# Kernel optimization log

Hardware: AMD Instinct MI355X
Metric: run time of the kernel (lower is better)

The kernel has to match this reference:

```python
import jax, jax.numpy as jnp
import numpy as np

B, T, C = 4, 2048, 2048
N_HEAD = 16
N_KV_HEAD = 4
N_REP = N_HEAD // N_KV_HEAD  # 4
HD = C // N_HEAD             # 128
FC_MULT = 1.0
EPS = 1e-12


def l2norm(x):
    return x / (jnp.linalg.norm(x, axis=-1, keepdims=True) + EPS)


def setup_inputs() -> dict:
    key = jax.random.key(0)
    k1, k2, k3, k4 = jax.random.split(key, 4)
    s = 1.0 / np.sqrt(C)
    return {
        "x": jax.random.normal(k1, (B, T, C), dtype=jnp.float32),
        "Wq": jax.random.normal(k2, (C, C), dtype=jnp.float32) * s,
        "Wkv": jax.random.normal(k3, (C, 2 * C // N_REP), dtype=jnp.float32) * s,
        "Wproj": jax.random.normal(k4, (C, C), dtype=jnp.float32) * s,
    }


def reference(x, Wq, Wkv, Wproj):
    kv_dim = C // N_REP  # 512
    q = FC_MULT * (x @ Wq)                     # [B,T,C]
    kv = FC_MULT * (x @ Wkv)                   # [B,T,2*kv_dim]
    k, v = kv[..., :kv_dim], kv[..., kv_dim:]
    # L2 prenorm over full projection dims (before head split), as in module
    q = l2norm(q)
    k = l2norm(k)
    # split heads; GQA without materializing repeated K/V
    q = q.reshape(B, T, N_KV_HEAD, N_REP, HD)  # [B,T,G,R,H]
    k = k.reshape(B, T, N_KV_HEAD, HD)         # [B,S,G,H]
    v = v.reshape(B, T, N_KV_HEAD, HD)
    scale = 1.0 / np.sqrt(HD)
    scores = jnp.einsum('btgrh,bsgh->bgrts', q, k) * scale  # [B,G,R,T,S]
    causal = jnp.tril(jnp.ones((T, T), dtype=bool))
    scores = jnp.where(causal, scores, -jnp.inf)
    att = jax.nn.softmax(scores, axis=-1)
    y = jnp.einsum('bgrts,bsgh->btgrh', att, v)  # [B,T,G,R,H]
    y = y.reshape(B, T, C)
    return FC_MULT * (y @ Wproj)
```

## Files before the change

kernel.cpp:

```cpp
#include <hip/hip_runtime.h>
#include <hip/hip_bf16.h>
#include <math.h>

#define B_   4
#define T_   2048
#define C_   2048
#define NH_  16
#define HD_  128
#define KVD_ 1024

typedef __attribute__((ext_vector_type(4))) float f32x4;
typedef __attribute__((ext_vector_type(16))) float f32x16;
typedef __attribute__((ext_vector_type(8))) short bf16x8;
typedef __attribute__((ext_vector_type(4))) unsigned int u32x4;

__device__ __forceinline__ void async_copy16(const __hip_bfloat16* g, __hip_bfloat16* l) {
  __builtin_amdgcn_global_load_lds((const __attribute__((address_space(1))) void*)g,
                                   (__attribute__((address_space(3))) void*)l,
                                   16, 0, 0);
}

__device__ __forceinline__ float bf2f(__hip_bfloat16 h) { return __bfloat162float(h); }

__device__ __forceinline__ unsigned int pkbf(float a, float b) {
  float2 f2; f2.x = a; f2.y = b;
  __hip_bfloat162 h2 = __float22bfloat162_rn(f2);
  return *reinterpret_cast<unsigned int*>(&h2);
}

__global__ __launch_bounds__(256) void f32_to_bf16_k(const float* __restrict__ src,
                                                     __hip_bfloat16* __restrict__ dst, int n4) {
  int i = blockIdx.x * 256 + threadIdx.x;
  if (i >= n4) return;
  float4 f = ((const float4*)src)[i];
  __hip_bfloat16 o[4] = {__float2bfloat16(f.x), __float2bfloat16(f.y),
                         __float2bfloat16(f.z), __float2bfloat16(f.w)};
  *(uint2*)(dst + (size_t)i * 4) = *(uint2*)o;
}

__global__ __launch_bounds__(256) void transpose_f32_bf16_k(const float* __restrict__ W,
                                                            __hip_bfloat16* __restrict__ WT,
                                                            int K, int N) {
  __shared__ float tile[32][33];
  int bx = blockIdx.x * 32;
  int by = blockIdx.y * 32;
  int tx = threadIdx.x, ty = threadIdx.y;
  for (int i = ty; i < 32; i += 8)
    tile[i][tx] = W[(size_t)(by + i) * N + (bx + tx)];
  __syncthreads();
  for (int i = ty; i < 32; i += 8)
    WT[(size_t)(bx + i) * K + (by + tx)] = __float2bfloat16(tile[tx][i]);
}

__global__ __launch_bounds__(256) void vtrans_k(const __hip_bfloat16* __restrict__ kv,
                                                __hip_bfloat16* __restrict__ vt) {
  __shared__ __hip_bfloat16 tile[32][33];
  int bg = blockIdx.z;
  int d0 = blockIdx.y * 32;
  int t0 = blockIdx.x * 32;
  int tx = threadIdx.x, ty = threadIdx.y;
  int b = bg >> 2, g = bg & 3;
  const __hip_bfloat16* src = kv + (size_t)b * T_ * KVD_ + 512 + g * HD_;
  for (int i = ty; i < 32; i += 8)
    tile[i][tx] = src[(size_t)(t0 + i) * KVD_ + d0 + tx];
  __syncthreads();
  __hip_bfloat16* dst = vt + (size_t)bg * HD_ * T_;
  int txp = (tx & ~12) | ((tx & 4) << 1) | ((tx & 8) >> 1);
  for (int i = ty; i < 32; i += 8)
    dst[(size_t)(d0 + i) * T_ + t0 + txp] = tile[tx][i];
}

template<int PER>
__global__ __launch_bounds__(256) void rownorm_k(__hip_bfloat16* __restrict__ buf,
                                                 int stride, float extra) {
  const int tid = threadIdx.x;
  __hip_bfloat16* p = buf + (size_t)blockIdx.x * stride;
  float v[PER];
  float ss = 0.f;
  #pragma unroll
  for (int e = 0; e < PER; ++e) { v[e] = bf2f(p[tid + e * 256]); ss += v[e] * v[e]; }
  #pragma unroll
  for (int off = 32; off >= 1; off >>= 1) ss += __shfl_xor(ss, off, 64);
  __shared__ float wsum[4];
  if ((tid & 63) == 0) wsum[tid >> 6] = ss;
  __syncthreads();
  float tot = wsum[0] + wsum[1] + wsum[2] + wsum[3];
  float sc = extra / (sqrtf(tot) + 1e-12f);
  #pragma unroll
  for (int e = 0; e < PER; ++e) p[tid + e * 256] = __float2bfloat16(v[e] * sc);
}

template<typename OutT>
__global__ __launch_bounds__(256) void gemm_bt_k(const __hip_bfloat16* __restrict__ A,
                                                 const __hip_bfloat16* __restrict__ BT,
                                                 OutT* __restrict__ Cc,
                                                 int M, int N, int K) {
  __shared__ alignas(16) __hip_bfloat16 As[128 * 32];
  __shared__ alignas(16) __hip_bfloat16 Bs[128 * 32];
  const int tid = threadIdx.x;
  const int bm = blockIdx.y * 128;
  const int bn = blockIdx.x * 128;
  const int wave = tid >> 6, lane = tid & 63;
  const int wr = (wave >> 1) * 64, wc = (wave & 1) * 64;
  const int lm = lane & 15, lk = (lane >> 4) * 8;
  const size_t Kz = (size_t)K;
  const __hip_bfloat16* a0 = A + (size_t)(bm + (tid >> 2)) * Kz + (size_t)((tid & 3) * 8);
  const __hip_bfloat16* b0 = BT + (size_t)(bn + (tid >> 2)) * Kz + (size_t)((tid & 3) * 8);
  const __hip_bfloat16* a1 = a0 + 64 * Kz;
  const __hip_bfloat16* b1 = b0 + 64 * Kz;
  f32x4 acc[4][4] = {};
  for (int k0 = 0; k0 < K; k0 += 32) {
    async_copy16(a0 + k0, As + tid * 8);
    async_copy16(a1 + k0, As + 2048 + tid * 8);
    async_copy16(b0 + k0, Bs + tid * 8);
    async_copy16(b1 + k0, Bs + 2048 + tid * 8);
    __syncthreads();
    bf16x8 af[4], bfr[4];
    #pragma unroll
    for (int t = 0; t < 4; ++t) {
      af[t]  = *(const bf16x8*)(As + (wr + t * 16 + lm) * 32 + lk);
      bfr[t] = *(const bf16x8*)(Bs + (wc + t * 16 + lm) * 32 + lk);
    }
    #pragma unroll
    for (int mt = 0; mt < 4; ++mt)
      #pragma unroll
      for (int nt = 0; nt < 4; ++nt)
        acc[mt][nt] = __builtin_amdgcn_mfma_f32_16x16x32_bf16(af[mt], bfr[nt], acc[mt][nt], 0, 0, 0);
    __syncthreads();
  }
  const int r0 = (lane >> 4) * 4;
  #pragma unroll
  for (int mt = 0; mt < 4; ++mt)
    #pragma unroll
    for (int nt = 0; nt < 4; ++nt)
      #pragma unroll
      for (int r = 0; r < 4; ++r) {
        int gr = bm + wr + mt * 16 + r0 + r;
        int gc = bn + wc + nt * 16 + lm;
        float v = acc[mt][nt][r];
        if constexpr (__is_same(OutT, float))
          Cc[(size_t)gr * N + gc] = v;
        else
          Cc[(size_t)gr * N + gc] = __float2bfloat16(v);
      }
}

__global__ __launch_bounds__(256, 2) void attn_k(const __hip_bfloat16* __restrict__ q,
                                                 const __hip_bfloat16* __restrict__ kv,
                                                 const __hip_bfloat16* __restrict__ vt,
                                                 __hip_bfloat16* __restrict__ y) {
  const int pp = blockIdx.x;
  const int h  = blockIdx.y;
  const int b  = blockIdx.z;
  const int g  = h >> 2;
  const int tid = threadIdx.x;
  const int wave = tid >> 6, lane = tid & 63;
  const int l31 = lane & 31, hi = lane >> 5;

  __shared__ alignas(16) __hip_bfloat16 Ks[2][64 * 128];
  __shared__ alignas(16) __hip_bfloat16 Vts[2][128 * 64];

  const __hip_bfloat16* kb = kv + (size_t)b * T_ * KVD_ + g * HD_;
  const __hip_bfloat16* vb = vt + (size_t)(b * 4 + g) * HD_ * T_;

  auto stage = [&](int buf, int jt) {
    const size_t j1 = (size_t)jt * 64;
    #pragma unroll
    for (int e = 0; e < 4; ++e) {
      int idx = tid + e * 256;
      int row = idx >> 4, c = idx & 15;
      async_copy16(kb + (j1 + row) * KVD_ + ((c ^ (row & 15)) * 8), Ks[buf] + idx * 8);
    }
    #pragma unroll
    for (int e = 0; e < 4; ++e) {
      int idx = tid + e * 256;
      int row = idx >> 3, c = idx & 7;
      async_copy16(vb + (size_t)row * T_ + j1 + ((c ^ (row & 7)) * 8), Vts[buf] + idx * 8);
    }
  };

  stage(0, 0);

  #pragma unroll
  for (int seg = 0; seg < 2; ++seg) {
    const int qt = seg ? pp : (15 - pp);
    const int qbase = qt * 128 + wave * 32;
    const int qmax = qbase + 31;
    const int ntiles = 2 * qt + 2;

    const __hip_bfloat16* qrow = q + ((size_t)b * T_ + qbase + l31) * C_ + h * HD_;
    bf16x8 qf[8];
    #pragma unroll
    for (int kc = 0; kc < 8; ++kc)
      qf[kc] = *(const bf16x8*)(qrow + kc * 16 + hi * 8);

    __syncthreads();

    f32x16 o_acc[4] = {};
    float l_acc = 0.f;

    for (int it = 0; it < ntiles; ++it) {
      const int cur = it & 1;
      if (it + 1 < ntiles) stage(cur ^ 1, it + 1);
      const int j0 = it * 64;
      if (j0 <= qmax) {
        f32x16 st0 = {}, st1 = {};
        __builtin_amdgcn_s_setprio(1);
        #pragma unroll
        for (int kc = 0; kc < 8; ++kc) {
          const int cs0 = (((2 * kc + hi) ^ (l31 & 15)) * 8);
          bf16x8 k0 = *(const bf16x8*)(Ks[cur] + l31 * 128 + cs0);
          bf16x8 k1 = *(const bf16x8*)(Ks[cur] + (32 + l31) * 128 + cs0);
          st0 = __builtin_amdgcn_mfma_f32_32x32x16_bf16(k0, qf[kc], st0, 0, 0, 0);
          st1 = __builtin_amdgcn_mfma_f32_32x32x16_bf16(k1, qf[kc], st1, 0, 0, 0);
        }
        __builtin_amdgcn_s_setprio(0);
        const int qd = qbase + l31 - j0;
        if (j0 + 63 <= qbase) {
          #pragma unroll
          for (int r = 0; r < 16; ++r) {
            float p0 = __expf(st0[r]);
            float p1 = __expf(st1[r]);
            st0[r] = p0; st1[r] = p1;
            l_acc += p0 + p1;
          }
        } else {
          #pragma unroll
          for (int r = 0; r < 16; ++r) {
            const int ofs = (r & 3) + 8 * (r >> 2) + 4 * hi;
            float p0 = (ofs <= qd) ? __expf(st0[r]) : 0.f;
            float p1 = (ofs + 32 <= qd) ? __expf(st1[r]) : 0.f;
            st0[r] = p0; st1[r] = p1;
            l_acc += p0 + p1;
          }
        }
        unsigned int W[8][2];
        #pragma unroll
        for (int q4 = 0; q4 < 4; ++q4) {
          W[q4][0]     = pkbf(st0[4 * q4 + 0], st0[4 * q4 + 1]);
          W[q4][1]     = pkbf(st0[4 * q4 + 2], st0[4 * q4 + 3]);
          W[4 + q4][0] = pkbf(st1[4 * q4 + 0], st1[4 * q4 + 1]);
          W[4 + q4][1] = pkbf(st1[4 * q4 + 2], st1[4 * q4 + 3]);
        }
        __builtin_amdgcn_s_setprio(1);
        #pragma unroll
        for (int kc = 0; kc < 4; ++kc) {
          u32x4 pw;
          pw[0] = W[2 * kc][0]; pw[1] = W[2 * kc][1];
          pw[2] = W[2 * kc + 1][0]; pw[3] = W[2 * kc + 1][1];
          bf16x8 pf = __builtin_bit_cast(bf16x8, pw);
          const int csv = (((2 * kc + hi) ^ (l31 & 7)) * 8);
          #pragma unroll
          for (int ct = 0; ct < 4; ++ct) {
            bf16x8 vf = *(const bf16x8*)(Vts[cur] + (ct * 32 + l31) * 64 + csv);
            o_acc[ct] = __builtin_amdgcn_mfma_f32_32x32x16_bf16(pf, vf, o_acc[ct], 0, 0, 0);
          }
        }
        __builtin_amdgcn_s_setprio(0);
      }
      __syncthreads();
    }

    if (seg == 0) stage(0, 0);

    float lsum = l_acc + __shfl_xor(l_acc, 32, 64);
    float oinv[16];
    #pragma unroll
    for (int r = 0; r < 16; ++r) {
      int row = (r & 3) + 8 * (r >> 2) + 4 * hi;
      oinv[r] = 1.0f / __shfl(lsum, row, 64);
    }
    __hip_bfloat16* yb = y + ((size_t)b * T_ + qbase) * C_ + h * HD_ + l31;
    #pragma unroll
    for (int ct = 0; ct < 4; ++ct)
      #pragma unroll
      for (int r = 0; r < 16; ++r) {
        int row = (r & 3) + 8 * (r >> 2) + 4 * hi;
        yb[(size_t)row * C_ + ct * 32] = __float2bfloat16(o_acc[ct][r] * oinv[r]);
      }
  }
}

extern "C" void kernel_launch(void* const* d_in, const int* in_sizes, int n_in,
                              void* d_out, int out_size, void* d_ws, size_t ws_size,
                              hipStream_t stream) {
  (void)in_sizes; (void)n_in; (void)out_size; (void)ws_size;
  const float* x     = (const float*)d_in[0];
  const float* Wq    = (const float*)d_in[1];
  const float* Wkv   = (const float*)d_in[2];
  const float* Wproj = (const float*)d_in[3];
  char* ws = (char*)d_ws;
  __hip_bfloat16* xb     = (__hip_bfloat16*)(ws);
  __hip_bfloat16* WqT    = (__hip_bfloat16*)(ws + 33554432);
  __hip_bfloat16* WkvT   = (__hip_bfloat16*)(ws + 41943040);
  __hip_bfloat16* WprojT = (__hip_bfloat16*)(ws + 46137344);
  __hip_bfloat16* qn     = (__hip_bfloat16*)(ws + 54525952);
  __hip_bfloat16* kvb    = (__hip_bfloat16*)(ws + 88080384);
  __hip_bfloat16* y      = xb;
  __hip_bfloat16* vt     = (__hip_bfloat16*)d_out;
  float* out             = (float*)d_out;

  f32_to_bf16_k<<<16384, 256, 0, stream>>>(x, xb, 4194304);
  transpose_f32_bf16_k<<<dim3(64, 64), dim3(32, 8), 0, stream>>>(Wq, WqT, 2048, 2048);
  transpose_f32_bf16_k<<<dim3(32, 64), dim3(32, 8), 0, stream>>>(Wkv, WkvT, 2048, 1024);
  transpose_f32_bf16_k<<<dim3(64, 64), dim3(32, 8), 0, stream>>>(Wproj, WprojT, 2048, 2048);
  gemm_bt_k<__hip_bfloat16><<<dim3(16, 64), 256, 0, stream>>>(xb, WqT, qn, 8192, 2048, 2048);
  gemm_bt_k<__hip_bfloat16><<<dim3(8, 64), 256, 0, stream>>>(xb, WkvT, kvb, 8192, 1024, 2048);
  rownorm_k<8><<<8192, 256, 0, stream>>>(qn, 2048, 0.08838834764831845f);
  rownorm_k<2><<<8192, 256, 0, stream>>>(kvb, 1024, 1.0f);
  vtrans_k<<<dim3(64, 4, 16), dim3(32, 8), 0, stream>>>(kvb, vt);
  attn_k<<<dim3(8, 16, 4), 256, 0, stream>>>(qn, kvb, vt, y);
  gemm_bt_k<float><<<dim3(16, 64), 256, 0, stream>>>(y, WprojT, out, 8192, 2048, 2048);
}
```

Before: 546.8 us.

## Replace GEMM with triple-buffered 128x256 tile kernel using async LDS prefetch

Replaces the single-buffered 128x128x32 bf16 GEMM with a 512-thread kernel that computes 128x256 tiles with K-step 64. It triple-buffers the LDS tiles via global_load_lds prefetching two steps ahead, and uses an XOR-swizzled LDS layout to avoid bank conflicts. It also splits the MFMA work into two halves, interleaving B-tile loads between them, and raises wave priority while the MFMAs run. The goal is to hide global memory latency and remove the barrier stalls of the old kernel. The cost is about 144KB of LDS per block and hand-written vmcnt waits that have to match the number of issued copies.

```diff
diff --git a/kernel.cpp b/kernel.cpp
--- a/kernel.cpp
+++ b/kernel.cpp
@@ -91,53 +91,114 @@
 }
 
 template<typename OutT>
-__global__ __launch_bounds__(256) void gemm_bt_k(const __hip_bfloat16* __restrict__ A,
-                                                 const __hip_bfloat16* __restrict__ BT,
-                                                 OutT* __restrict__ Cc,
-                                                 int M, int N, int K) {
-  __shared__ alignas(16) __hip_bfloat16 As[128 * 32];
-  __shared__ alignas(16) __hip_bfloat16 Bs[128 * 32];
-  const int tid = threadIdx.x;
-  const int bm = blockIdx.y * 128;
-  const int bn = blockIdx.x * 128;
+__global__ __launch_bounds__(512, 2) void gemm3_k(const __hip_bfloat16* __restrict__ A,
+                                                  const __hip_bfloat16* __restrict__ BT,
+                                                  OutT* __restrict__ Cc,
+                                                  int M, int N, int K) {
+  __shared__ alignas(16) __hip_bfloat16 As[3][128 * 64];
+  __shared__ alignas(16) __hip_bfloat16 Bs[3][256 * 64];
+  const int tid  = threadIdx.x;
+  const int bm   = blockIdx.y * 128;
+  const int bn   = blockIdx.x * 256;
   const int wave = tid >> 6, lane = tid & 63;
-  const int wr = (wave >> 1) * 64, wc = (wave & 1) * 64;
-  const int lm = lane & 15, lk = (lane >> 4) * 8;
+  const int wm = wave >> 2, wn = wave & 3;
+  const int lm = lane & 15, quad = lane >> 4;
   const size_t Kz = (size_t)K;
-  const __hip_bfloat16* a0 = A + (size_t)(bm + (tid >> 2)) * Kz + (size_t)((tid & 3) * 8);
-  const __hip_bfloat16* b0 = BT + (size_t)(bn + (tid >> 2)) * Kz + (size_t)((tid & 3) * 8);
-  const __hip_bfloat16* a1 = a0 + 64 * Kz;
-  const __hip_bfloat16* b1 = b0 + 64 * Kz;
+  const int NT = K >> 6;
+
+  const int srow = tid >> 3;
+  const int csw  = ((tid & 7) ^ (srow & 7)) * 8;
+  const __hip_bfloat16* aSrc0 = A  + (size_t)(bm + srow) * Kz + csw;
+  const __hip_bfloat16* aSrc1 = A  + (size_t)(bm + 64 + srow) * Kz + csw;
+  const __hip_bfloat16* bSrc0 = BT + (size_t)(bn + srow) * Kz + csw;
+  const __hip_bfloat16* bSrc1 = BT + (size_t)(bn + 64 + srow) * Kz + csw;
+  const __hip_bfloat16* bSrc2 = BT + (size_t)(bn + 128 + srow) * Kz + csw;
+  const __hip_bfloat16* bSrc3 = BT + (size_t)(bn + 192 + srow) * Kz + csw;
+
+  auto stageA = [&](int slot, int koff) {
+    async_copy16(aSrc0 + koff, As[slot] + tid * 8);
+    async_copy16(aSrc1 + koff, As[slot] + (512 + tid) * 8);
+  };
+  auto stageB0 = [&](int slot, int koff) {
+    async_copy16(bSrc0 + koff, Bs[slot] + tid * 8);
+  };
+  auto stageB123 = [&](int slot, int koff) {
+    async_copy16(bSrc1 + koff, Bs[slot] + (512 + tid) * 8);
+    async_copy16(bSrc2 + koff, Bs[slot] + (1024 + tid) * 8);
+    async_copy16(bSrc3 + koff, Bs[slot] + (1536 + tid) * 8);
+  };
+
+  const int ch0 = ((quad) ^ (lm & 7)) * 8;
+  const int ch1 = ((4 + quad) ^ (lm & 7)) * 8;
+  const int arow = wm * 64 + lm;
+  const int brow = wn * 64 + lm;
+
   f32x4 acc[4][4] = {};
-  for (int k0 = 0; k0 < K; k0 += 32) {
-    async_copy16(a0 + k0, As + tid * 8);
-    async_copy16(a1 + k0, As + 2048 + tid * 8);
-    async_copy16(b0 + k0, Bs + tid * 8);
-    async_copy16(b1 + k0, Bs + 2048 + tid * 8);
-    __syncthreads();
-    bf16x8 af[4], bfr[4];
-    #pragma unroll
-    for (int t = 0; t < 4; ++t) {
-      af[t]  = *(const bf16x8*)(As + (wr + t * 16 + lm) * 32 + lk);
-      bfr[t] = *(const bf16x8*)(Bs + (wc + t * 16 + lm) * 32 + lk);
-    }
-    #pragma unroll
-    for (int mt = 0; mt < 4; ++mt)
+
+  stageA(0, 0); stageB0(0, 0); stageB123(0, 0);
+  if (NT > 1) { stageA(1, 64); stageB0(1, 64); stageB123(1, 64); }
+
+  int s = 0;
+  for (int t = 0; t < NT; ++t) {
+    const int sn = (s + 2 > 2) ? (s - 1) : (s + 2);
+    const bool pre = (t + 2) < NT;
+    const int koff = (t + 2) * 64;
+    if (t + 1 < NT) asm volatile("s_waitcnt vmcnt(6)" ::: "memory");
+    else            asm volatile("s_waitcnt vmcnt(0)" ::: "memory");
+    __builtin_amdgcn_s_barrier();
+    bf16x8 af[4][2], bf0[2][2];
+    #pragma unroll
+    for (int mf = 0; mf < 4; ++mf) {
+      af[mf][0] = *(const bf16x8*)(As[s] + (arow + mf * 16) * 64 + ch0);
+      af[mf][1] = *(const bf16x8*)(As[s] + (arow + mf * 16) * 64 + ch1);
+    }
+    #pragma unroll
+    for (int nf = 0; nf < 2; ++nf) {
+      bf0[nf][0] = *(const bf16x8*)(Bs[s] + (brow + nf * 16) * 64 + ch0);
+      bf0[nf][1] = *(const bf16x8*)(Bs[s] + (brow + nf * 16) * 64 + ch1);
+    }
+    if (pre) { stageA(sn, koff); stageB0(sn, koff); }
+    __builtin_amdgcn_s_barrier();
+    __builtin_amdgcn_s_setprio(1);
+    #pragma unroll
+    for (int mf = 0; mf < 4; ++mf)
       #pragma unroll
-      for (int nt = 0; nt < 4; ++nt)
-        acc[mt][nt] = __builtin_amdgcn_mfma_f32_16x16x32_bf16(af[mt], bfr[nt], acc[mt][nt], 0, 0, 0);
-    __syncthreads();
+      for (int nf = 0; nf < 2; ++nf) {
+        acc[mf][nf] = __builtin_amdgcn_mfma_f32_16x16x32_bf16(af[mf][0], bf0[nf][0], acc[mf][nf], 0, 0, 0);
+        acc[mf][nf] = __builtin_amdgcn_mfma_f32_16x16x32_bf16(af[mf][1], bf0[nf][1], acc[mf][nf], 0, 0, 0);
+      }
+    __builtin_amdgcn_s_setprio(0);
+    __builtin_amdgcn_s_barrier();
+    bf16x8 bf1[2][2];
+    #pragma unroll
+    for (int nf = 0; nf < 2; ++nf) {
+      bf1[nf][0] = *(const bf16x8*)(Bs[s] + (brow + (nf + 2) * 16) * 64 + ch0);
+      bf1[nf][1] = *(const bf16x8*)(Bs[s] + (brow + (nf + 2) * 16) * 64 + ch1);
+    }
+    if (pre) stageB123(sn, koff);
+    __builtin_amdgcn_s_barrier();
+    __builtin_amdgcn_s_setprio(1);
+    #pragma unroll
+    for (int mf = 0; mf < 4; ++mf)
+      #pragma unroll
+      for (int nf = 0; nf < 2; ++nf) {
+        acc[mf][nf + 2] = __builtin_amdgcn_mfma_f32_16x16x32_bf16(af[mf][0], bf1[nf][0], acc[mf][nf + 2], 0, 0, 0);
+        acc[mf][nf + 2] = __builtin_amdgcn_mfma_f32_16x16x32_bf16(af[mf][1], bf1[nf][1], acc[mf][nf + 2], 0, 0, 0);
+      }
+    __builtin_amdgcn_s_setprio(0);
+    s = (s == 2) ? 0 : s + 1;
   }
-  const int r0 = (lane >> 4) * 4;
-  #pragma unroll
-  for (int mt = 0; mt < 4; ++mt)
-    #pragma unroll
-    for (int nt = 0; nt < 4; ++nt)
+
+  const int r0 = quad * 4;
+  #pragma unroll
+  for (int mf = 0; mf < 4; ++mf)
+    #pragma unroll
+    for (int nf = 0; nf < 4; ++nf)
       #pragma unroll
       for (int r = 0; r < 4; ++r) {
-        int gr = bm + wr + mt * 16 + r0 + r;
-        int gc = bn + wc + nt * 16 + lm;
-        float v = acc[mt][nt][r];
+        int gr = bm + wm * 64 + mf * 16 + r0 + r;
+        int gc = bn + wn * 64 + nf * 16 + lm;
+        float v = acc[mf][nf][r];
         if constexpr (__is_same(OutT, float))
           Cc[(size_t)gr * N + gc] = v;
         else
@@ -304,11 +365,11 @@
   transpose_f32_bf16_k<<<dim3(64, 64), dim3(32, 8), 0, stream>>>(Wq, WqT, 2048, 2048);
   transpose_f32_bf16_k<<<dim3(32, 64), dim3(32, 8), 0, stream>>>(Wkv, WkvT, 2048, 1024);
   transpose_f32_bf16_k<<<dim3(64, 64), dim3(32, 8), 0, stream>>>(Wproj, WprojT, 2048, 2048);
-  gemm_bt_k<__hip_bfloat16><<<dim3(16, 64), 256, 0, stream>>>(xb, WqT, qn, 8192, 2048, 2048);
-  gemm_bt_k<__hip_bfloat16><<<dim3(8, 64), 256, 0, stream>>>(xb, WkvT, kvb, 8192, 1024, 2048);
+  gemm3_k<__hip_bfloat16><<<dim3(8, 64), 512, 0, stream>>>(xb, WqT, qn, 8192, 2048, 2048);
+  gemm3_k<__hip_bfloat16><<<dim3(4, 64), 512, 0, stream>>>(xb, WkvT, kvb, 8192, 1024, 2048);
   rownorm_k<8><<<8192, 256, 0, stream>>>(qn, 2048, 0.08838834764831845f);
   rownorm_k<2><<<8192, 256, 0, stream>>>(kvb, 1024, 1.0f);
   vtrans_k<<<dim3(64, 4, 16), dim3(32, 8), 0, stream>>>(kvb, vt);
   attn_k<<<dim3(8, 16, 4), 256, 0, stream>>>(qn, kvb, vt, y);
-  gemm_bt_k<float><<<dim3(16, 64), 256, 0, stream>>>(y, WprojT, out, 8192, 2048, 2048);
-}
+  gemm3_k<float><<<dim3(8, 64), 512, 0, stream>>>(y, WprojT, out, 8192, 2048, 2048);
+}
```

Measured after the change: 466.9 us. -14.6%, faster.
